# Performance work log

Measured on AMD Instinct MI355X. Metric: run time of the kernel, lower is better.

Reference implementation:

```python
import jax, jax.numpy as jnp
import numpy as np

N_ANGLES = 180
N_DETECTORS = 256


def _bilinear_sample(img, x, y):
    """Bilinear sample img[y, x]; zero outside. img: [H, W]; x, y: any shape."""
    H, W = img.shape
    x0 = jnp.floor(x)
    y0 = jnp.floor(y)
    xi = x0.astype(jnp.int32)
    yi = y0.astype(jnp.int32)
    wx = x - x0
    wy = y - y0

    def get(ix, iy):
        valid = (ix >= 0) & (ix < W) & (iy >= 0) & (iy < H)
        ixc = jnp.clip(ix, 0, W - 1)
        iyc = jnp.clip(iy, 0, H - 1)
        return jnp.where(valid, img[iyc, ixc], jnp.zeros((), img.dtype))

    v00 = get(xi, yi)
    v01 = get(xi + 1, yi)
    v10 = get(xi, yi + 1)
    v11 = get(xi + 1, yi + 1)
    return (v00 * (1.0 - wx) + v01 * wx) * (1.0 - wy) + (v10 * (1.0 - wx) + v11 * wx) * wy


def setup_inputs() -> dict:
    key = jax.random.key(0)
    inputs = jax.random.uniform(key, (8, 256, 256, 1), dtype=jnp.float32)
    return {"inputs": inputs}


def reference(inputs):
    # Parallel-beam forward Radon transform (forwardproject).
    # inputs: [B, H, W, 1] image batch -> sinogram [B, n_angles, n_detectors, 1]
    B, H, W, _ = inputs.shape
    A, D = N_ANGLES, N_DETECTORS
    T = H  # integration samples along each ray

    theta = jnp.linspace(0.0, jnp.pi, A, endpoint=False, dtype=inputs.dtype)
    cos_t = jnp.cos(theta)[:, None, None]  # [A,1,1]
    sin_t = jnp.sin(theta)[:, None, None]

    s = (jnp.arange(D, dtype=inputs.dtype) - (D - 1) / 2.0)[None, :, None]  # detector offsets
    t = (jnp.arange(T, dtype=inputs.dtype) - (T - 1) / 2.0)[None, None, :]  # along-ray offsets

    cx = (W - 1) / 2.0
    cy = (H - 1) / 2.0
    # sample coords for every (angle, detector, ray-step): [A, D, T]
    x = cx + s * cos_t - t * sin_t
    y = cy + s * sin_t + t * cos_t

    imgs = inputs[..., 0]  # [B, H, W]
    vals = jax.vmap(lambda im: _bilinear_sample(im, x, y))(imgs)  # [B, A, D, T]
    sino = vals.sum(axis=-1)  # ray integral (unit step length)
    return sino[..., None]  # [B, A, D, 1]
```

## Files before the change

kernel.cpp:

```cpp
#include <hip/hip_runtime.h>
#include <math.h>

#define NA    180
#define HB    9
#define KB    29
#define PC    262
#define PR    264
#define TROWS 12
#define TSZ   (PC * TROWS)
#define TSZ4  (TSZ / 2)
#define OUTN  (8 * NA * 256)

typedef _Float16 h2  __attribute__((ext_vector_type(2)));
typedef _Float16 h4  __attribute__((ext_vector_type(4)));
typedef __fp16   hf2 __attribute__((ext_vector_type(2)));

__device__ __forceinline__ h2 pkrtz(float a, float b) {
    hf2 t = __builtin_amdgcn_cvt_pkrtz(a, b);
    return __builtin_bit_cast(h2, t);
}
__device__ __forceinline__ float fdot2f(h2 a, h2 b, float c) {
#if __has_builtin(__builtin_amdgcn_fdot2)
    return __builtin_amdgcn_fdot2(__builtin_bit_cast(hf2, a),
                                  __builtin_bit_cast(hf2, b), c, false);
#else
    return c + (float)a.x * (float)b.x + (float)a.y * (float)b.y;
#endif
}
__device__ __forceinline__ float imc(const float* im, int y, int x) {
    return ((unsigned)y < 256u && (unsigned)x < 256u) ? im[(y << 8) + x] : 0.0f;
}

__global__ __launch_bounds__(256) void prep_kernel(
    const float* __restrict__ img, uint2* __restrict__ P0,
    uint2* __restrict__ P1, float* __restrict__ out, float* __restrict__ tab)
{
    const int tid = threadIdx.x;
    const int row = blockIdx.x;
    const int mb  = blockIdx.y;

    if (mb == 0) {
        for (int i = row * 256 + tid; i < OUTN; i += PR * 256) out[i] = 0.0f;
    }
    if (mb == 1 && row == 0 && tid < NA) {
        const float theta = (float)tid * ((float)M_PI / (float)NA);
        tab[tid]      = cosf(theta);
        tab[tid + NA] = sinf(theta);
    }

    const int bg = mb & 1;
    const float* im0 = img + ((size_t)(bg * 4) << 16);
    const int v = row - 3;

    if (mb < 2) {
        uint2* dst = P0 + (size_t)(bg * PR + row) * PC;
        for (int j = tid; j < PC; j += 256) {
            const int u = j - 2;
            h4 t = {};
            if (j < 261) {
                t[0] = (_Float16)imc(im0,             v, u);
                t[1] = (_Float16)imc(im0 + (1 << 16), v, u);
                t[2] = (_Float16)imc(im0 + (2 << 16), v, u);
                t[3] = (_Float16)imc(im0 + (3 << 16), v, u);
            }
            dst[j] = __builtin_bit_cast(uint2, t);
        }
    } else {
        uint2* dst = P1 + (size_t)(bg * PR + row) * PC;
        for (int j = tid; j < PC; j += 256) {
            const int u = j - 2;
            h4 t = {};
            if (j < 261) {
                t[0] = (_Float16)imc(im0,             u, v);
                t[1] = (_Float16)imc(im0 + (1 << 16), u, v);
                t[2] = (_Float16)imc(im0 + (2 << 16), u, v);
                t[3] = (_Float16)imc(im0 + (3 << 16), u, v);
            }
            dst[j] = __builtin_bit_cast(uint2, t);
        }
    }
}

#define SAMPLE(JV, UV, VPV, A0, A1, A2, A3)                                   \
    {                                                                         \
        const float ucl = fminf(fmaxf((UV), -1.5f), 257.5f);                  \
        const float uf = floorf(ucl);                                         \
        const float wu = ucl - uf;                                            \
        const float vf = floorf(VPV);                                         \
        const float wv = (VPV) - vf;                                          \
        const float vfc = fminf(fmaxf(vf, -1.0f), 9.0f);                      \
        const int idx = (int)fmaf(vfc, (float)PC, uf) + (PC + 2);             \
        const h4 r00 = __builtin_bit_cast(h4, s_tile[idx]);                   \
        const h4 r01 = __builtin_bit_cast(h4, s_tile[idx + 1]);               \
        const h4 r10 = __builtin_bit_cast(h4, s_tile[idx + PC]);              \
        const h4 r11 = __builtin_bit_cast(h4, s_tile[idx + PC + 1]);          \
        const h2 wv2 = pkrtz(wv, wv);                                         \
        const h4 wv4 = __builtin_shufflevector(wv2, wv2, 0, 1, 0, 1);         \
        const h4 V0 = (r10 - r00) * wv4 + r00;                                \
        const h4 V1 = (r11 - r01) * wv4 + r01;                                \
        h2 wu2 = pkrtz(1.0f - wu, wu);                                        \
        wu2 = ((unsigned)(JV) < span) ? wu2 : hz;                             \
        A0 = fdot2f(__builtin_shufflevector(V0, V1, 0, 4), wu2, A0);          \
        A1 = fdot2f(__builtin_shufflevector(V0, V1, 1, 5), wu2, A1);          \
        A2 = fdot2f(__builtin_shufflevector(V0, V1, 2, 6), wu2, A2);          \
        A3 = fdot2f(__builtin_shufflevector(V0, V1, 3, 7), wu2, A3);          \
    }

template<bool MODEX>
__device__ __forceinline__ void radon_body(
    const uint2* __restrict__ Pbase,
    float* __restrict__ out, const float* __restrict__ tab,
    uint2* s_tile, int tid, int b0, int p, int gi)
{
    const int lo = -2 + p * HB;

    {
        const uint4* src = (const uint4*)(Pbase + (size_t)(lo + 2) * PC);
        uint4* dst = (uint4*)s_tile;
        for (int i = tid; i < TSZ4; i += 256) dst[i] = src[i];
    }
    __syncthreads();

    const float detf = (float)tid - 127.5f;
    const float lof = (float)lo;
    const h2 hz = {};

    for (int g = 0; g < 7; ++g) {
        const int ai = gi * 7 + g;
        int a;
        if (MODEX) { if (ai >= 89) break; a = 46 + ai; }
        else       { a = (ai <= 45) ? ai : 89 + ai; }

        const float c = tab[a];
        const float s = tab[a + NA];

        const float xc = 127.5f + detf * c + 127.5f * s;
        const float yc = 127.5f + detf * s - 127.5f * c;

        const float ucst = MODEX ? yc : xc;
        const float vcst = MODEX ? xc : yc;
        const float du   = MODEX ? c  : -s;
        const float dv   = MODEX ? -s : c;

        const float inv = 1.0f / dv;
        const float f1 = (lof - vcst) * inv;
        const float f2 = (lof + (float)HB - vcst) * inv;
        const float fmn = fminf(f1, f2);
        const float fmx = fmaxf(f1, f2);
        int kmin, kend;
        if (dv > 0.0f) { kmin = (int)ceilf(fmn);      kend = (int)ceilf(fmx); }
        else           { kmin = (int)floorf(fmn) + 1; kend = (int)floorf(fmx) + 1; }

        const int len = kend - kmin;
        const int jlo = max(0, -kmin);
        const int jhi = min(len, 256 - kmin);
        const int spani = max(0, jhi - jlo);
        if (!__any(spani > 0)) continue;
        const unsigned span = (unsigned)spani;

        const int kstart = kmin + jlo;
        const int Lmax = (int)((float)HB * fabsf(inv)) + 2;

        float u  = fmaf((float)kstart, du, ucst);
        float vp = fmaf((float)kstart, dv, vcst - lof);
        const float du2 = du + du, dv2 = dv + dv;

        float a0 = 0.f, a1 = 0.f, a2 = 0.f, a3 = 0.f;
        float b0a = 0.f, b1a = 0.f, b2a = 0.f, b3a = 0.f;

        int j = 0;
        for (; j + 1 < Lmax; j += 2) {
            SAMPLE(j,     u,      vp,      a0, a1, a2, a3);
            SAMPLE(j + 1, u + du, vp + dv, b0a, b1a, b2a, b3a);
            u += du2; vp += dv2;
        }
        if (j < Lmax) SAMPLE(j, u, vp, a0, a1, a2, a3);

        if (spani > 0) {
            float* o = &out[((b0 * NA + a) << 8) + tid];
            atomicAdd(o,                 a0 + b0a);
            atomicAdd(o + (NA << 8),     a1 + b1a);
            atomicAdd(o + 2 * (NA << 8), a2 + b2a);
            atomicAdd(o + 3 * (NA << 8), a3 + b3a);
        }
    }
}

__global__ __launch_bounds__(256, 6) void radon_kernel(
    const uint2* __restrict__ P0, const uint2* __restrict__ P1,
    float* __restrict__ out, const float* __restrict__ tab)
{
    __shared__ uint2 s_tile[TSZ];
    const int tid = threadIdx.x;
    const int bg  = blockIdx.x;
    const int p   = blockIdx.y;
    const int gid = blockIdx.z;
    const int b0  = bg * 4;
    if (gid < 13)
        radon_body<false>(P0 + (size_t)bg * PR * PC, out, tab, s_tile, tid, b0, p, gid);
    else
        radon_body<true>(P1 + (size_t)bg * PR * PC, out, tab, s_tile, tid, b0, p, gid - 13);
}

extern "C" void kernel_launch(void* const* d_in, const int* in_sizes, int n_in,
                              void* d_out, int out_size, void* d_ws, size_t ws_size,
                              hipStream_t stream) {
    const float* img = (const float*)d_in[0];
    float* out = (float*)d_out;

    uint2* P0 = (uint2*)d_ws;
    uint2* P1 = P0 + (size_t)2 * PR * PC;
    float* tab = (float*)(P1 + (size_t)2 * PR * PC);

    prep_kernel<<<dim3(PR, 4), 256, 0, stream>>>(img, P0, P1, out, tab);
    radon_kernel<<<dim3(2, KB, 26), 256, 0, stream>>>(P0, P1, out, tab);
}
```

Baseline: 106.2 us.

## Use fewer angles per block and unroll ray sampling by four

Cuts the angles each block handles from 7 to 4, raising the grid from 26 to 46 angle-groups per tile row. The aim is more blocks in flight and better load balance across CUs. The inner ray loop is also unrolled by four with four independent accumulator sets, exposing more LDS-load and dot-product ILP. In exchange, each block reloads its shared tile for fewer angles, and the extra accumulators raise register pressure.

```diff
diff --git a/kernel.cpp b/kernel.cpp
--- a/kernel.cpp
+++ b/kernel.cpp
@@ -10,6 +10,8 @@
 #define TSZ   (PC * TROWS)
 #define TSZ4  (TSZ / 2)
 #define OUTN  (8 * NA * 256)
+#define APG   4
+#define NG    23
 
 typedef _Float16 h2  __attribute__((ext_vector_type(2)));
 typedef _Float16 h4  __attribute__((ext_vector_type(4)));
@@ -101,7 +103,7 @@
         h2 wu2 = pkrtz(1.0f - wu, wu);                                        \
         wu2 = ((unsigned)(JV) < span) ? wu2 : hz;                             \
         A0 = fdot2f(__builtin_shufflevector(V0, V1, 0, 4), wu2, A0);          \
-        A1 = fdot2f(__builtin_shufflevector(V0, V1, 1, 5), wu2, A1);          \
+        A1 = fdot2f(__builtin_shufflevector(V0, V1, 1, 5), wu2, A1);         \
         A2 = fdot2f(__builtin_shufflevector(V0, V1, 2, 6), wu2, A2);          \
         A3 = fdot2f(__builtin_shufflevector(V0, V1, 3, 7), wu2, A3);          \
     }
@@ -125,11 +127,11 @@
     const float lof = (float)lo;
     const h2 hz = {};
 
-    for (int g = 0; g < 7; ++g) {
-        const int ai = gi * 7 + g;
+    for (int g = 0; g < APG; ++g) {
+        const int ai = gi * APG + g;
         int a;
         if (MODEX) { if (ai >= 89) break; a = 46 + ai; }
-        else       { a = (ai <= 45) ? ai : 89 + ai; }
+        else       { if (ai >= 91) break; a = (ai <= 45) ? ai : 89 + ai; }
 
         const float c = tab[a];
         const float s = tab[a + NA];
@@ -164,24 +166,35 @@
         float u  = fmaf((float)kstart, du, ucst);
         float vp = fmaf((float)kstart, dv, vcst - lof);
         const float du2 = du + du, dv2 = dv + dv;
+        const float du3 = du2 + du, dv3 = dv2 + dv;
+        const float du4 = du2 + du2, dv4 = dv2 + dv2;
 
         float a0 = 0.f, a1 = 0.f, a2 = 0.f, a3 = 0.f;
-        float b0a = 0.f, b1a = 0.f, b2a = 0.f, b3a = 0.f;
+        float e0 = 0.f, e1 = 0.f, e2 = 0.f, e3 = 0.f;
+        float c0 = 0.f, c1 = 0.f, c2 = 0.f, c3 = 0.f;
+        float d0 = 0.f, d1 = 0.f, d2 = 0.f, d3 = 0.f;
 
         int j = 0;
+        for (; j + 3 < Lmax; j += 4) {
+            SAMPLE(j,     u,        vp,        a0, a1, a2, a3);
+            SAMPLE(j + 1, u + du,   vp + dv,   e0, e1, e2, e3);
+            SAMPLE(j + 2, u + du2,  vp + dv2,  c0, c1, c2, c3);
+            SAMPLE(j + 3, u + du3,  vp + dv3,  d0, d1, d2, d3);
+            u += du4; vp += dv4;
+        }
         for (; j + 1 < Lmax; j += 2) {
             SAMPLE(j,     u,      vp,      a0, a1, a2, a3);
-            SAMPLE(j + 1, u + du, vp + dv, b0a, b1a, b2a, b3a);
+            SAMPLE(j + 1, u + du, vp + dv, e0, e1, e2, e3);
             u += du2; vp += dv2;
         }
         if (j < Lmax) SAMPLE(j, u, vp, a0, a1, a2, a3);
 
         if (spani > 0) {
             float* o = &out[((b0 * NA + a) << 8) + tid];
-            atomicAdd(o,                 a0 + b0a);
-            atomicAdd(o + (NA << 8),     a1 + b1a);
-            atomicAdd(o + 2 * (NA << 8), a2 + b2a);
-            atomicAdd(o + 3 * (NA << 8), a3 + b3a);
+            atomicAdd(o,                 (a0 + c0) + (e0 + d0));
+            atomicAdd(o + (NA << 8),     (a1 + c1) + (e1 + d1));
+            atomicAdd(o + 2 * (NA << 8), (a2 + c2) + (e2 + d2));
+            atomicAdd(o + 3 * (NA << 8), (a3 + c3) + (e3 + d3));
         }
     }
 }
@@ -196,10 +209,10 @@
     const int p   = blockIdx.y;
     const int gid = blockIdx.z;
     const int b0  = bg * 4;
-    if (gid < 13)
+    if (gid < NG)
         radon_body<false>(P0 + (size_t)bg * PR * PC, out, tab, s_tile, tid, b0, p, gid);
     else
-        radon_body<true>(P1 + (size_t)bg * PR * PC, out, tab, s_tile, tid, b0, p, gid - 13);
+        radon_body<true>(P1 + (size_t)bg * PR * PC, out, tab, s_tile, tid, b0, p, gid - NG);
 }
 
 extern "C" void kernel_launch(void* const* d_in, const int* in_sizes, int n_in,
@@ -213,5 +226,5 @@
     float* tab = (float*)(P1 + (size_t)2 * PR * PC);
 
     prep_kernel<<<dim3(PR, 4), 256, 0, stream>>>(img, P0, P1, out, tab);
-    radon_kernel<<<dim3(2, KB, 26), 256, 0, stream>>>(P0, P1, out, tab);
-}
+    radon_kernel<<<dim3(2, KB, 2 * NG), 256, 0, stream>>>(P0, P1, out, tab);
+}
```

Measured after the change: 100.4 us. 5.4% less time.
